# Kernel optimization log

Measured on AMD Instinct MI355X. Metric: run time of the kernel, lower is better.

The kernel has to match this reference:

```python
import jax, jax.numpy as jnp
import numpy as np

EPS = 1e-5

def setup_inputs() -> dict:
    key = jax.random.key(0)
    kx, kq, kp = jax.random.split(key, 3)
    B, T, d = 4, 4096, 512
    x = jax.random.normal(kx, (B, T, d), dtype=jnp.float32)
    mask = jnp.tril(jnp.ones((T, T), dtype=jnp.int32))  # causal 0/1 mask
    gamma = jnp.ones((d,), dtype=jnp.float32)
    beta = jnp.zeros((d,), dtype=jnp.float32)
    Wqkv = jax.random.normal(kq, (d, 3 * d), dtype=jnp.float32) / np.sqrt(d)
    Wproj = jax.random.normal(kp, (d, d), dtype=jnp.float32) / np.sqrt(d)
    return {"x": x, "mask": mask, "gamma": gamma, "beta": beta, "Wqkv": Wqkv, "Wproj": Wproj}

def reference(x, mask, gamma, beta, Wqkv, Wproj):
    B, T, C = x.shape
    # LayerNorm over last dim
    mu = jnp.mean(x, axis=-1, keepdims=True)
    var = jnp.mean(jnp.square(x - mu), axis=-1, keepdims=True)
    xn = (x - mu) * jax.lax.rsqrt(var + EPS) * gamma + beta
    # QKV projection (no bias)
    qkv = xn @ Wqkv  # [B,T,3C]
    q, k, v = jnp.split(qkv, 3, axis=-1)
    scale = 1.0 / np.sqrt(C)
    dist = jnp.einsum('btc,bsc->bts', q, k) * scale  # [B,T,T]
    dist = jnp.where(mask[:T, :T] == 0, -jnp.inf, dist)
    attn = jax.nn.softmax(dist, axis=-1)
    out = jnp.einsum('bts,bsc->btc', attn, v)
    return out @ Wproj
```

## Files before the change

kernel.cpp:

```cpp
#include <hip/hip_runtime.h>

typedef short bf16x8 __attribute__((ext_vector_type(8)));
typedef float f32x4 __attribute__((ext_vector_type(4)));

#define AS1 __attribute__((address_space(1)))
#define AS3 __attribute__((address_space(3)))

__device__ __forceinline__ void async16(const void* g, void* l) {
    __builtin_amdgcn_global_load_lds((AS1 unsigned*)(unsigned long long)g,
                                     (AS3 unsigned*)l, 16, 0, 0);
}

__device__ __forceinline__ unsigned short f2bf(float f) {
    unsigned u = __builtin_bit_cast(unsigned, f);
    u += 0x7fffu + ((u >> 16) & 1u);
    return (unsigned short)(u >> 16);
}
__device__ __forceinline__ float bf2f(unsigned short s) {
    unsigned u = ((unsigned)s) << 16;
    return __builtin_bit_cast(float, u);
}

__global__ __launch_bounds__(256) void ln_bf16_kernel(
    const float* __restrict__ x, const float* __restrict__ gamma,
    const float* __restrict__ beta, unsigned short* __restrict__ xn, int nrows)
{
    int row = blockIdx.x * 4 + (threadIdx.x >> 6);
    int lane = threadIdx.x & 63;
    if (row >= nrows) return;
    const float4* xr = (const float4*)(x + (size_t)row * 512);
    float4 a = xr[lane], b = xr[lane + 64];
    float s = a.x + a.y + a.z + a.w + b.x + b.y + b.z + b.w;
    #pragma unroll
    for (int m = 1; m < 64; m <<= 1) s += __shfl_xor(s, m);
    float mu = s * (1.0f / 512.0f);
    float dx[8] = {a.x - mu, a.y - mu, a.z - mu, a.w - mu,
                   b.x - mu, b.y - mu, b.z - mu, b.w - mu};
    float ss = 0.f;
    #pragma unroll
    for (int i = 0; i < 8; ++i) ss += dx[i] * dx[i];
    #pragma unroll
    for (int m = 1; m < 64; m <<= 1) ss += __shfl_xor(ss, m);
    float rstd = rsqrtf(ss * (1.0f / 512.0f) + 1e-5f);
    const float4* gp = (const float4*)gamma;
    const float4* bp = (const float4*)beta;
    float4 g0 = gp[lane], g1 = gp[lane + 64], b0 = bp[lane], b1 = bp[lane + 64];
    float y[8];
    y[0] = dx[0] * rstd * g0.x + b0.x; y[1] = dx[1] * rstd * g0.y + b0.y;
    y[2] = dx[2] * rstd * g0.z + b0.z; y[3] = dx[3] * rstd * g0.w + b0.w;
    y[4] = dx[4] * rstd * g1.x + b1.x; y[5] = dx[5] * rstd * g1.y + b1.y;
    y[6] = dx[6] * rstd * g1.z + b1.z; y[7] = dx[7] * rstd * g1.w + b1.w;
    ushort4* orow = (ushort4*)(xn + (size_t)row * 512);
    orow[lane]      = make_ushort4(f2bf(y[0]), f2bf(y[1]), f2bf(y[2]), f2bf(y[3]));
    orow[lane + 64] = make_ushort4(f2bf(y[4]), f2bf(y[5]), f2bf(y[6]), f2bf(y[7]));
}

__global__ __launch_bounds__(256) void transpose_w(
    const float* __restrict__ in, unsigned short* __restrict__ outT, int R, int Cd)
{
    __shared__ float tile[64][65];
    int r0 = blockIdx.x * 64, c0 = blockIdx.y * 64;
    int lr = threadIdx.x >> 6, lc = threadIdx.x & 63;
    #pragma unroll
    for (int i = 0; i < 16; ++i) {
        int r = i * 4 + lr;
        tile[r][lc] = in[(size_t)(r0 + r) * Cd + c0 + lc];
    }
    __syncthreads();
    #pragma unroll
    for (int i = 0; i < 16; ++i) {
        int r = i * 4 + lr;
        outT[(size_t)(c0 + r) * R + r0 + lc] = f2bf(tile[lc][r]);
    }
}

__global__ __launch_bounds__(256) void transpose_v(
    const unsigned short* __restrict__ vraw, unsigned short* __restrict__ vtp)
{
    __shared__ unsigned short tile[64][72];
    int b = blockIdx.z;
    int t0 = blockIdx.x * 64, c0 = blockIdx.y * 64;
    int lr = threadIdx.x >> 6, lc = threadIdx.x & 63;
    const unsigned short* src = vraw + (size_t)(b * 4096 + t0) * 512 + c0;
    #pragma unroll
    for (int i = 0; i < 16; ++i) {
        int r = i * 4 + lr;
        tile[r][lc] = src[(size_t)r * 512 + lc];
    }
    __syncthreads();
    #pragma unroll
    for (int i = 0; i < 16; ++i) {
        int r = i * 4 + lr;
        int c = c0 + r;
        int jt = (t0 >> 5) + (lc >> 5);
        int tl = lc & 31;
        int x = tl >> 3;
        int slot = c * 4 + ((x ^ (c >> 1)) & 3);
        vtp[((size_t)(b * 128 + jt)) * 16384 + slot * 8 + (tl & 7)] = tile[lc][r];
    }
}

__global__ __launch_bounds__(256) void gemm_bt(
    const unsigned short* __restrict__ A, const unsigned short* __restrict__ Bt,
    void* __restrict__ Cp, int M, int N, int K, int lda, int ldb, int ldc, int outBf16)
{
    __shared__ unsigned short As[128 * 64];
    __shared__ unsigned short Bs[128 * 64];
    const int tid = threadIdx.x;
    const int w = tid >> 6, lane = tid & 63, quad = lane >> 4, l15 = lane & 15;
    const int wm = w >> 1, wn = w & 1;
    const size_t m0 = (size_t)blockIdx.x * 128, n0 = (size_t)blockIdx.y * 128;
    f32x4 zero = {0.f, 0.f, 0.f, 0.f};
    f32x4 acc[4][4];
    #pragma unroll
    for (int i = 0; i < 4; ++i)
        #pragma unroll
        for (int j = 0; j < 4; ++j) acc[i][j] = zero;

    for (int k0 = 0; k0 < K; k0 += 64) {
        __syncthreads();
        #pragma unroll
        for (int r = 0; r < 4; ++r) {
            int s = r * 256 + w * 64 + lane;
            int row = s >> 3, x = s & 7, g = x ^ (row & 7);
            async16(A + (m0 + row) * lda + k0 + g * 8,
                    (char*)As + (size_t)(r * 256 + w * 64) * 16);
        }
        #pragma unroll
        for (int r = 0; r < 4; ++r) {
            int s = r * 256 + w * 64 + lane;
            int row = s >> 3, x = s & 7, g = x ^ (row & 7);
            async16(Bt + (n0 + row) * ldb + k0 + g * 8,
                    (char*)Bs + (size_t)(r * 256 + w * 64) * 16);
        }
        __syncthreads();
        #pragma unroll
        for (int ks = 0; ks < 2; ++ks) {
            bf16x8 af[4], bf[4];
            int cc = ks * 4 + quad;
            #pragma unroll
            for (int mt = 0; mt < 4; ++mt) {
                int row = wm * 64 + mt * 16 + l15;
                int x = cc ^ (row & 7);
                af[mt] = *(const bf16x8*)(As + row * 64 + x * 8);
            }
            #pragma unroll
            for (int nt = 0; nt < 4; ++nt) {
                int row = wn * 64 + nt * 16 + l15;
                int x = cc ^ (row & 7);
                bf[nt] = *(const bf16x8*)(Bs + row * 64 + x * 8);
            }
            #pragma unroll
            for (int mt = 0; mt < 4; ++mt)
                #pragma unroll
                for (int nt = 0; nt < 4; ++nt)
                    acc[mt][nt] = __builtin_amdgcn_mfma_f32_16x16x32_bf16(
                        af[mt], bf[nt], acc[mt][nt], 0, 0, 0);
        }
    }
    #pragma unroll
    for (int mt = 0; mt < 4; ++mt)
        #pragma unroll
        for (int nt = 0; nt < 4; ++nt)
            #pragma unroll
            for (int r = 0; r < 4; ++r) {
                size_t grow = m0 + wm * 64 + mt * 16 + quad * 4 + r;
                size_t gcol = n0 + wn * 64 + nt * 16 + l15;
                float v = acc[mt][nt][r];
                if (outBf16) ((unsigned short*)Cp)[grow * ldc + gcol] = f2bf(v);
                else         ((float*)Cp)[grow * ldc + gcol] = v;
            }
}

__global__ __launch_bounds__(256, 2) void attn_kernel(
    const unsigned short* __restrict__ qk,
    const unsigned short* __restrict__ vtp,
    unsigned short* __restrict__ ph0, unsigned short* __restrict__ ph1,
    float* __restrict__ lp)
{
    __shared__ unsigned short Ks[32 * 512];
    __shared__ unsigned short Vs[32 * 512];
    unsigned short* Ps = Ks;

    const int id = blockIdx.x;
    const int cu = id & 255, hi = id >> 8;
    const int b = cu & 3;
    const int q = hi ? (63 - (cu >> 2)) : (cu >> 2);
    const int h = hi;

    const int jt0 = h ? (q + 1) : 0;
    const int jtN = h ? (2 * q + 2) : (q + 1);

    const int tid = threadIdx.x, w = tid >> 6, lane = tid & 63;
    const int quad = lane >> 4, l15 = lane & 15;
    const float scale = 0.04419417382415922f;
    f32x4 zero = {0.f, 0.f, 0.f, 0.f};

    const unsigned short* kbase = qk + (size_t)(b * 4096) * 1024 + 512;
    const unsigned short* vbase = vtp + (size_t)(b * 128) * 16384;
    unsigned short* dst = h ? ph1 : ph0;

    bf16x8 qf[16];
    {
        const unsigned short* qb =
            qk + (size_t)(b * 4096 + q * 64 + w * 16 + l15) * 1024;
        #pragma unroll
        for (int ks = 0; ks < 16; ++ks)
            qf[ks] = *(const bf16x8*)(qb + ks * 32 + quad * 8);
    }
    f32x4 o[32];
    #pragma unroll
    for (int i = 0; i < 32; ++i) o[i] = zero;
    float li[4] = {0.f, 0.f, 0.f, 0.f};

    for (int jt = jt0; jt < jtN; ++jt) {
        __syncthreads();
        {
            const unsigned short* kg = kbase + (size_t)jt * 32 * 1024;
            #pragma unroll
            for (int rnd = 0; rnd < 8; ++rnd) {
                int s = rnd * 256 + tid;
                int row = s >> 6, xx = s & 63;
                int g = (xx & ~7) | ((xx ^ row) & 7);
                async16(kg + (size_t)row * 1024 + g * 8,
                        (char*)Ks + (size_t)(rnd * 256 + w * 64) * 16);
            }
            const unsigned short* vg = vbase + (size_t)jt * 16384;
            #pragma unroll
            for (int rnd = 0; rnd < 8; ++rnd) {
                int s = rnd * 256 + tid;
                async16(vg + (size_t)s * 8,
                        (char*)Vs + (size_t)(rnd * 256 + w * 64) * 16);
            }
        }
        __syncthreads();

        f32x4 sa[2];
        sa[0] = zero; sa[1] = zero;
        #pragma unroll
        for (int ks = 0; ks < 16; ++ks) {
            int cc = ks * 4 + quad;
            #pragma unroll
            for (int nt = 0; nt < 2; ++nt) {
                int jr = nt * 16 + l15;
                int xg = (cc & ~7) | ((cc ^ jr) & 7);
                bf16x8 kf = *(const bf16x8*)(Ks + jr * 512 + xg * 8);
                sa[nt] = __builtin_amdgcn_mfma_f32_16x16x32_bf16(
                    qf[ks], kf, sa[nt], 0, 0, 0);
            }
        }
        const int trow = q * 64 + w * 16 + quad * 4;
        unsigned short pb[4][2];
        #pragma unroll
        for (int r = 0; r < 4; ++r) {
            #pragma unroll
            for (int nt = 0; nt < 2; ++nt) {
                int col = jt * 32 + nt * 16 + l15;
                float sv = sa[nt][r] * scale;
                float pv = __expf(fminf(sv, 60.f));
                if (col > trow + r) pv = 0.f;
                li[r] += pv;
                pb[r][nt] = f2bf(pv);
            }
        }
        __syncthreads();
        #pragma unroll
        for (int r = 0; r < 4; ++r)
            #pragma unroll
            for (int nt = 0; nt < 2; ++nt)
                Ps[w * 640 + (quad * 4 + r) * 40 + nt * 16 + l15] = pb[r][nt];

        bf16x8 pf = *(const bf16x8*)(Ps + w * 640 + l15 * 40 + quad * 8);
        #pragma unroll
        for (int ct = 0; ct < 32; ++ct) {
            int cch = ct * 16 + l15;
            int slot = cch * 4 + ((quad ^ (cch >> 1)) & 3);
            bf16x8 vf = *(const bf16x8*)(Vs + slot * 8);
            o[ct] = __builtin_amdgcn_mfma_f32_16x16x32_bf16(pf, vf, o[ct], 0, 0, 0);
        }
    }

    #pragma unroll
    for (int r = 0; r < 4; ++r) {
        float s = li[r];
        s += __shfl_xor(s, 1);
        s += __shfl_xor(s, 2);
        s += __shfl_xor(s, 4);
        s += __shfl_xor(s, 8);
        if (l15 == 0)
            lp[h * 16384 + b * 4096 + q * 64 + w * 16 + quad * 4 + r] = s;
    }
    unsigned short* ob = dst + (size_t)(b * 4096 + q * 64 + w * 16) * 512;
    #pragma unroll
    for (int ct = 0; ct < 32; ++ct)
        #pragma unroll
        for (int r = 0; r < 4; ++r)
            ob[(size_t)(quad * 4 + r) * 512 + ct * 16 + l15] = f2bf(o[ct][r]);
}

__global__ __launch_bounds__(256) void combine_kernel(
    const unsigned short* __restrict__ ph0, const unsigned short* __restrict__ ph1,
    const float* __restrict__ lp, unsigned short* __restrict__ att)
{
    int t = blockIdx.x * 4 + (threadIdx.x >> 6);
    int lane = threadIdx.x & 63;
    float inv = 1.0f / (lp[t] + lp[16384 + t]);
    const ushort4* pa = (const ushort4*)(ph0 + (size_t)t * 512 + lane * 8);
    const ushort4* pb = (const ushort4*)(ph1 + (size_t)t * 512 + lane * 8);
    ushort4* po = (ushort4*)(att + (size_t)t * 512 + lane * 8);
    #pragma unroll
    for (int i = 0; i < 2; ++i) {
        ushort4 a = pa[i], b = pb[i];
        po[i] = make_ushort4(
            f2bf((bf2f(a.x) + bf2f(b.x)) * inv),
            f2bf((bf2f(a.y) + bf2f(b.y)) * inv),
            f2bf((bf2f(a.z) + bf2f(b.z)) * inv),
            f2bf((bf2f(a.w) + bf2f(b.w)) * inv));
    }
}

extern "C" void kernel_launch(void* const* d_in, const int* in_sizes, int n_in,
                              void* d_out, int out_size, void* d_ws, size_t ws_size,
                              hipStream_t stream)
{
    const float* x     = (const float*)d_in[0];
    const float* gamma = (const float*)d_in[2];
    const float* beta  = (const float*)d_in[3];
    const float* Wqkv  = (const float*)d_in[4];
    const float* Wproj = (const float*)d_in[5];
    float* out = (float*)d_out;

    char* ws = (char*)d_ws;
    unsigned short* qk     = (unsigned short*)(ws);
    unsigned short* vraw   = (unsigned short*)(ws + 33554432);
    unsigned short* vtp    = (unsigned short*)(ws + 50331648);
    unsigned short* xn     = (unsigned short*)(ws + 67108864);
    unsigned short* wqkvT  = (unsigned short*)(ws + 83886080);
    unsigned short* wprojT = (unsigned short*)(ws + 85458944);
    unsigned short* ph0    = xn;
    unsigned short* ph1    = vraw;
    float*          lp     = (float*)wqkvT;
    unsigned short* att    = vtp;

    ln_bf16_kernel<<<4096, 256, 0, stream>>>(x, gamma, beta, xn, 16384);
    transpose_w<<<dim3(8, 24), 256, 0, stream>>>(Wqkv, wqkvT, 512, 1536);
    transpose_w<<<dim3(8, 8), 256, 0, stream>>>(Wproj, wprojT, 512, 512);
    gemm_bt<<<dim3(128, 8), 256, 0, stream>>>(xn, wqkvT, qk,
                                              16384, 1024, 512, 512, 512, 1024, 1);
    gemm_bt<<<dim3(128, 4), 256, 0, stream>>>(xn, wqkvT + 1024 * 512, vraw,
                                              16384, 512, 512, 512, 512, 512, 1);
    transpose_v<<<dim3(64, 8, 4), 256, 0, stream>>>(vraw, vtp);
    attn_kernel<<<512, 256, 0, stream>>>(qk, vtp, ph0, ph1, lp);
    combine_kernel<<<4096, 256, 0, stream>>>(ph0, ph1, lp, att);
    gemm_bt<<<dim3(128, 4), 256, 0, stream>>>(att, wprojT, out,
                                              16384, 512, 512, 512, 512, 512, 0);
}
```

Measured before the change: 396.2 us.

## Restructure attention into 128-row tiles with 4-way KV split and double-buffered LDS

Rewrites the attention kernel to use 512-thread blocks that each handle a 128-query tile. The key range is split into four parts, and each block processes two work items chosen by reversed indexing to balance the causal load. K and V tiles are double-buffered, so async loads of the next tile overlap compute on the current one. The PV product is split across waves by output column rather than by query row, which cuts per-wave accumulator registers. The combine kernel now sums four partial outputs and uses the output buffer as scratch, adding memory traffic and relying on the final GEMM to overwrite it.

After: 436.9 us. 10.3% more time.

```diff
diff --git a/kernel.cpp b/kernel.cpp
--- a/kernel.cpp
+++ b/kernel.cpp
@@ -172,150 +172,172 @@
             }
 }
 
-__global__ __launch_bounds__(256, 2) void attn_kernel(
+__global__ __launch_bounds__(512, 2) void attn_kernel(
     const unsigned short* __restrict__ qk,
     const unsigned short* __restrict__ vtp,
     unsigned short* __restrict__ ph0, unsigned short* __restrict__ ph1,
+    unsigned short* __restrict__ ph2, unsigned short* __restrict__ ph3,
     float* __restrict__ lp)
 {
-    __shared__ unsigned short Ks[32 * 512];
-    __shared__ unsigned short Vs[32 * 512];
-    unsigned short* Ps = Ks;
-
-    const int id = blockIdx.x;
-    const int cu = id & 255, hi = id >> 8;
-    const int b = cu & 3;
-    const int q = hi ? (63 - (cu >> 2)) : (cu >> 2);
-    const int h = hi;
-
-    const int jt0 = h ? (q + 1) : 0;
-    const int jtN = h ? (2 * q + 2) : (q + 1);
+    __shared__ unsigned short Ks[2][32 * 512];
+    __shared__ unsigned short Vs[2][32 * 512];
+    __shared__ unsigned short Ps[128 * 40];
 
     const int tid = threadIdx.x, w = tid >> 6, lane = tid & 63;
     const int quad = lane >> 4, l15 = lane & 15;
     const float scale = 0.04419417382415922f;
     f32x4 zero = {0.f, 0.f, 0.f, 0.f};
 
-    const unsigned short* kbase = qk + (size_t)(b * 4096) * 1024 + 512;
-    const unsigned short* vbase = vtp + (size_t)(b * 128) * 16384;
-    unsigned short* dst = h ? ph1 : ph0;
-
-    bf16x8 qf[16];
-    {
-        const unsigned short* qb =
-            qk + (size_t)(b * 4096 + q * 64 + w * 16 + l15) * 1024;
-        #pragma unroll
-        for (int ks = 0; ks < 16; ++ks)
-            qf[ks] = *(const bf16x8*)(qb + ks * 32 + quad * 8);
-    }
-    f32x4 o[32];
-    #pragma unroll
-    for (int i = 0; i < 32; ++i) o[i] = zero;
-    float li[4] = {0.f, 0.f, 0.f, 0.f};
-
-    for (int jt = jt0; jt < jtN; ++jt) {
+    #pragma unroll 1
+    for (int half = 0; half < 2; ++half) {
+        const int j = half ? (511 - (int)blockIdx.x) : (int)blockIdx.x;
+        const int q = 31 - (j >> 4);
+        const int b = (j >> 2) & 3;
+        const int part = j & 3;
+        const int ntile = q + 1;
+        const int jt0 = part * ntile, jtN = jt0 + ntile;
+
+        const unsigned short* kbase = qk + (size_t)(b * 4096) * 1024 + 512;
+        const unsigned short* vbase = vtp + (size_t)(b * 128) * 16384;
+
+        bf16x8 qf[16];
+        {
+            const unsigned short* qb =
+                qk + (size_t)(b * 4096 + q * 128 + w * 16 + l15) * 1024;
+            #pragma unroll
+            for (int ks = 0; ks < 16; ++ks)
+                qf[ks] = *(const bf16x8*)(qb + ks * 32 + quad * 8);
+        }
+        f32x4 o[8][4];
+        #pragma unroll
+        for (int i = 0; i < 8; ++i)
+            #pragma unroll
+            for (int d = 0; d < 4; ++d) o[i][d] = zero;
+        float li[4] = {0.f, 0.f, 0.f, 0.f};
+
+        #define STAGE(BUF, T)                                                     \
+        {                                                                         \
+            const unsigned short* kg = kbase + (size_t)(T) * 32 * 1024;           \
+            _Pragma("unroll")                                                     \
+            for (int rnd = 0; rnd < 4; ++rnd) {                                   \
+                int s = rnd * 512 + tid;                                          \
+                int row = s >> 6, xx = s & 63;                                    \
+                int g = (xx & ~7) | ((xx ^ row) & 7);                             \
+                async16(kg + (size_t)row * 1024 + g * 8,                          \
+                        (char*)(&Ks[BUF][0]) + (size_t)(rnd * 512 + w * 64) * 16);\
+            }                                                                     \
+            const unsigned short* vg = vbase + (size_t)(T) * 16384;               \
+            _Pragma("unroll")                                                     \
+            for (int rnd = 0; rnd < 4; ++rnd) {                                   \
+                int s = rnd * 512 + tid;                                          \
+                async16(vg + (size_t)s * 8,                                       \
+                        (char*)(&Vs[BUF][0]) + (size_t)(rnd * 512 + w * 64) * 16);\
+            }                                                                     \
+        }
+
+        STAGE(0, jt0);
         __syncthreads();
-        {
-            const unsigned short* kg = kbase + (size_t)jt * 32 * 1024;
-            #pragma unroll
-            for (int rnd = 0; rnd < 8; ++rnd) {
-                int s = rnd * 256 + tid;
-                int row = s >> 6, xx = s & 63;
-                int g = (xx & ~7) | ((xx ^ row) & 7);
-                async16(kg + (size_t)row * 1024 + g * 8,
-                        (char*)Ks + (size_t)(rnd * 256 + w * 64) * 16);
-            }
-            const unsigned short* vg = vbase + (size_t)jt * 16384;
-            #pragma unroll
-            for (int rnd = 0; rnd < 8; ++rnd) {
-                int s = rnd * 256 + tid;
-                async16(vg + (size_t)s * 8,
-                        (char*)Vs + (size_t)(rnd * 256 + w * 64) * 16);
-            }
-        }
-        __syncthreads();
-
-        f32x4 sa[2];
-        sa[0] = zero; sa[1] = zero;
-        #pragma unroll
-        for (int ks = 0; ks < 16; ++ks) {
-            int cc = ks * 4 + quad;
-            #pragma unroll
-            for (int nt = 0; nt < 2; ++nt) {
-                int jr = nt * 16 + l15;
-                int xg = (cc & ~7) | ((cc ^ jr) & 7);
-                bf16x8 kf = *(const bf16x8*)(Ks + jr * 512 + xg * 8);
-                sa[nt] = __builtin_amdgcn_mfma_f32_16x16x32_bf16(
-                    qf[ks], kf, sa[nt], 0, 0, 0);
-            }
-        }
-        const int trow = q * 64 + w * 16 + quad * 4;
-        unsigned short pb[4][2];
+        int cur = 0;
+
+        #pragma unroll 1
+        for (int t = jt0; t < jtN; ++t) {
+            if (t + 1 < jtN) STAGE(cur ^ 1, t + 1);
+
+            f32x4 sa[2];
+            sa[0] = zero; sa[1] = zero;
+            #pragma unroll
+            for (int ks = 0; ks < 16; ++ks) {
+                int cc = ks * 4 + quad;
+                #pragma unroll
+                for (int nt = 0; nt < 2; ++nt) {
+                    int jr = nt * 16 + l15;
+                    int xg = (cc & ~7) | ((cc ^ jr) & 7);
+                    bf16x8 kf = *(const bf16x8*)(&Ks[cur][jr * 512 + xg * 8]);
+                    sa[nt] = __builtin_amdgcn_mfma_f32_16x16x32_bf16(
+                        qf[ks], kf, sa[nt], 0, 0, 0);
+                }
+            }
+            const int trow = q * 128 + w * 16 + quad * 4;
+            #pragma unroll
+            for (int r = 0; r < 4; ++r) {
+                #pragma unroll
+                for (int nt = 0; nt < 2; ++nt) {
+                    int col = t * 32 + nt * 16 + l15;
+                    float sv = sa[nt][r] * scale;
+                    float pv = __expf(fminf(sv, 60.f));
+                    if (col > trow + r) pv = 0.f;
+                    li[r] += pv;
+                    Ps[(w * 16 + quad * 4 + r) * 40 + nt * 16 + l15] = f2bf(pv);
+                }
+            }
+            asm volatile("s_waitcnt lgkmcnt(0)" ::: "memory");
+            __builtin_amdgcn_s_barrier();
+
+            bf16x8 vfr[4];
+            #pragma unroll
+            for (int df = 0; df < 4; ++df) {
+                int cch = (w * 4 + df) * 16 + l15;
+                int slot = cch * 4 + ((quad ^ (cch >> 1)) & 3);
+                vfr[df] = *(const bf16x8*)(&Vs[cur][slot * 8]);
+            }
+            #pragma unroll
+            for (int qi = 0; qi < 8; ++qi) {
+                bf16x8 pa = *(const bf16x8*)(&Ps[(qi * 16 + l15) * 40 + quad * 8]);
+                #pragma unroll
+                for (int df = 0; df < 4; ++df)
+                    o[qi][df] = __builtin_amdgcn_mfma_f32_16x16x32_bf16(
+                        pa, vfr[df], o[qi][df], 0, 0, 0);
+            }
+            __syncthreads();
+            cur ^= 1;
+        }
+        #undef STAGE
+
         #pragma unroll
         for (int r = 0; r < 4; ++r) {
-            #pragma unroll
-            for (int nt = 0; nt < 2; ++nt) {
-                int col = jt * 32 + nt * 16 + l15;
-                float sv = sa[nt][r] * scale;
-                float pv = __expf(fminf(sv, 60.f));
-                if (col > trow + r) pv = 0.f;
-                li[r] += pv;
-                pb[r][nt] = f2bf(pv);
-            }
-        }
-        __syncthreads();
-        #pragma unroll
-        for (int r = 0; r < 4; ++r)
-            #pragma unroll
-            for (int nt = 0; nt < 2; ++nt)
-                Ps[w * 640 + (quad * 4 + r) * 40 + nt * 16 + l15] = pb[r][nt];
-
-        bf16x8 pf = *(const bf16x8*)(Ps + w * 640 + l15 * 40 + quad * 8);
-        #pragma unroll
-        for (int ct = 0; ct < 32; ++ct) {
-            int cch = ct * 16 + l15;
-            int slot = cch * 4 + ((quad ^ (cch >> 1)) & 3);
-            bf16x8 vf = *(const bf16x8*)(Vs + slot * 8);
-            o[ct] = __builtin_amdgcn_mfma_f32_16x16x32_bf16(pf, vf, o[ct], 0, 0, 0);
-        }
-    }
-
-    #pragma unroll
-    for (int r = 0; r < 4; ++r) {
-        float s = li[r];
-        s += __shfl_xor(s, 1);
-        s += __shfl_xor(s, 2);
-        s += __shfl_xor(s, 4);
-        s += __shfl_xor(s, 8);
-        if (l15 == 0)
-            lp[h * 16384 + b * 4096 + q * 64 + w * 16 + quad * 4 + r] = s;
-    }
-    unsigned short* ob = dst + (size_t)(b * 4096 + q * 64 + w * 16) * 512;
-    #pragma unroll
-    for (int ct = 0; ct < 32; ++ct)
-        #pragma unroll
-        for (int r = 0; r < 4; ++r)
-            ob[(size_t)(quad * 4 + r) * 512 + ct * 16 + l15] = f2bf(o[ct][r]);
+            float s = li[r];
+            s += __shfl_xor(s, 1);
+            s += __shfl_xor(s, 2);
+            s += __shfl_xor(s, 4);
+            s += __shfl_xor(s, 8);
+            if (l15 == 0)
+                lp[part * 16384 + b * 4096 + q * 128 + w * 16 + quad * 4 + r] = s;
+        }
+        unsigned short* dst = (part == 0) ? ph0 : (part == 1) ? ph1
+                            : (part == 2) ? ph2 : ph3;
+        unsigned short* ob = dst + (size_t)(b * 4096 + q * 128) * 512 + w * 64;
+        #pragma unroll
+        for (int qi = 0; qi < 8; ++qi)
+            #pragma unroll
+            for (int df = 0; df < 4; ++df)
+                #pragma unroll
+                for (int r = 0; r < 4; ++r)
+                    ob[(size_t)(qi * 16 + quad * 4 + r) * 512 + df * 16 + l15] =
+                        f2bf(o[qi][df][r]);
+    }
 }
 
 __global__ __launch_bounds__(256) void combine_kernel(
     const unsigned short* __restrict__ ph0, const unsigned short* __restrict__ ph1,
+    const unsigned short* __restrict__ ph2, const unsigned short* __restrict__ ph3,
     const float* __restrict__ lp, unsigned short* __restrict__ att)
 {
     int t = blockIdx.x * 4 + (threadIdx.x >> 6);
     int lane = threadIdx.x & 63;
-    float inv = 1.0f / (lp[t] + lp[16384 + t]);
+    float inv = 1.0f / (lp[t] + lp[16384 + t] + lp[32768 + t] + lp[49152 + t]);
     const ushort4* pa = (const ushort4*)(ph0 + (size_t)t * 512 + lane * 8);
     const ushort4* pb = (const ushort4*)(ph1 + (size_t)t * 512 + lane * 8);
+    const ushort4* pc = (const ushort4*)(ph2 + (size_t)t * 512 + lane * 8);
+    const ushort4* pd = (const ushort4*)(ph3 + (size_t)t * 512 + lane * 8);
     ushort4* po = (ushort4*)(att + (size_t)t * 512 + lane * 8);
     #pragma unroll
     for (int i = 0; i < 2; ++i) {
-        ushort4 a = pa[i], b = pb[i];
+        ushort4 a = pa[i], b = pb[i], c = pc[i], d = pd[i];
         po[i] = make_ushort4(
-            f2bf((bf2f(a.x) + bf2f(b.x)) * inv),
-            f2bf((bf2f(a.y) + bf2f(b.y)) * inv),
-            f2bf((bf2f(a.z) + bf2f(b.z)) * inv),
-            f2bf((bf2f(a.w) + bf2f(b.w)) * inv));
+            f2bf((bf2f(a.x) + bf2f(b.x) + bf2f(c.x) + bf2f(d.x)) * inv),
+            f2bf((bf2f(a.y) + bf2f(b.y) + bf2f(c.y) + bf2f(d.y)) * inv),
+            f2bf((bf2f(a.z) + bf2f(b.z) + bf2f(c.z) + bf2f(d.z)) * inv),
+            f2bf((bf2f(a.w) + bf2f(b.w) + bf2f(c.w) + bf2f(d.w)) * inv));
     }
 }
 
@@ -339,6 +361,8 @@
     unsigned short* wprojT = (unsigned short*)(ws + 85458944);
     unsigned short* ph0    = xn;
     unsigned short* ph1    = vraw;
+    unsigned short* ph2    = (unsigned short*)out;
+    unsigned short* ph3    = (unsigned short*)out + (size_t)16384 * 512;
     float*          lp     = (float*)wqkvT;
     unsigned short* att    = vtp;
 
@@ -350,8 +374,8 @@
     gemm_bt<<<dim3(128, 4), 256, 0, stream>>>(xn, wqkvT + 1024 * 512, vraw,
                                               16384, 512, 512, 512, 512, 512, 1);
     transpose_v<<<dim3(64, 8, 4), 256, 0, stream>>>(vraw, vtp);
-    attn_kernel<<<512, 256, 0, stream>>>(qk, vtp, ph0, ph1, lp);
-    combine_kernel<<<4096, 256, 0, stream>>>(ph0, ph1, lp, att);
+    attn_kernel<<<256, 512, 0, stream>>>(qk, vtp, ph0, ph1, ph2, ph3, lp);
+    combine_kernel<<<4096, 256, 0, stream>>>(ph0, ph1, ph2, ph3, lp, att);
     gemm_bt<<<dim3(128, 4), 256, 0, stream>>>(att, wprojT, out,
                                               16384, 512, 512, 512, 512, 512, 0);
 }
```

## Repartition PV matmul so each wave owns a head-dim slice across all query rows

Applied to the files above, without the earlier changes.

The P·V stage is reorganised so each wave computes a 128-wide slice of the output dimension for all 64 query rows, instead of all 512 columns for its own 16 rows. This lets each wave load only a quarter of the V tile from LDS and reuse each V fragment across four P fragments. P therefore moves to its own shared buffer visible to every wave, with a barrier after it is written, and the old reuse of the K buffer plus the extra pre-write sync is dropped. K/V async-load address math is also hoisted out of the loop. The cost is more LDS, which may affect the two-blocks-per-CU occupancy target.

Result: faster. 362.6 us (-8.5%).

```diff
diff --git a/kernel.cpp b/kernel.cpp
--- a/kernel.cpp
+++ b/kernel.cpp
@@ -180,7 +180,7 @@
 {
     __shared__ unsigned short Ks[32 * 512];
     __shared__ unsigned short Vs[32 * 512];
-    unsigned short* Ps = Ks;
+    __shared__ unsigned short Ps[64 * 40];
 
     const int id = blockIdx.x;
     const int cu = id & 255, hi = id >> 8;
@@ -200,6 +200,12 @@
     const unsigned short* vbase = vtp + (size_t)(b * 128) * 16384;
     unsigned short* dst = h ? ph1 : ph0;
 
+    const int gE = (lane & ~7) | ((lane ^ w) & 7);
+    const int gO = (lane & ~7) | ((lane ^ (w + 4)) & 7);
+    const size_t kOffE = (size_t)w * 1024 + (size_t)gE * 8;
+    const size_t kOffO = (size_t)(w + 4) * 1024 + (size_t)gO * 8;
+    const size_t vOff  = (size_t)tid * 8;
+
     bf16x8 qf[16];
     {
         const unsigned short* qb =
@@ -208,30 +214,29 @@
         for (int ks = 0; ks < 16; ++ks)
             qf[ks] = *(const bf16x8*)(qb + ks * 32 + quad * 8);
     }
-    f32x4 o[32];
-    #pragma unroll
-    for (int i = 0; i < 32; ++i) o[i] = zero;
+    f32x4 o[4][8];
+    #pragma unroll
+    for (int i = 0; i < 4; ++i)
+        #pragma unroll
+        for (int d = 0; d < 8; ++d) o[i][d] = zero;
     float li[4] = {0.f, 0.f, 0.f, 0.f};
 
     for (int jt = jt0; jt < jtN; ++jt) {
         __syncthreads();
         {
-            const unsigned short* kg = kbase + (size_t)jt * 32 * 1024;
-            #pragma unroll
-            for (int rnd = 0; rnd < 8; ++rnd) {
-                int s = rnd * 256 + tid;
-                int row = s >> 6, xx = s & 63;
-                int g = (xx & ~7) | ((xx ^ row) & 7);
-                async16(kg + (size_t)row * 1024 + g * 8,
-                        (char*)Ks + (size_t)(rnd * 256 + w * 64) * 16);
-            }
-            const unsigned short* vg = vbase + (size_t)jt * 16384;
-            #pragma unroll
-            for (int rnd = 0; rnd < 8; ++rnd) {
-                int s = rnd * 256 + tid;
-                async16(vg + (size_t)s * 8,
+            const unsigned short* kg = kbase + (size_t)jt * 32768;
+            #pragma unroll
+            for (int rr = 0; rr < 4; ++rr) {
+                async16(kg + (size_t)(2 * rr) * 4096 + kOffE,
+                        (char*)Ks + (size_t)((2 * rr) * 256 + w * 64) * 16);
+                async16(kg + (size_t)(2 * rr) * 4096 + kOffO,
+                        (char*)Ks + (size_t)((2 * rr + 1) * 256 + w * 64) * 16);
+            }
+            const unsigned short* vg = vbase + (size_t)jt * 16384 + vOff;
+            #pragma unroll
+            for (int rnd = 0; rnd < 8; ++rnd)
+                async16(vg + (size_t)rnd * 2048,
                         (char*)Vs + (size_t)(rnd * 256 + w * 64) * 16);
-            }
         }
         __syncthreads();
 
@@ -250,7 +255,6 @@
             }
         }
         const int trow = q * 64 + w * 16 + quad * 4;
-        unsigned short pb[4][2];
         #pragma unroll
         for (int r = 0; r < 4; ++r) {
             #pragma unroll
@@ -260,23 +264,29 @@
                 float pv = __expf(fminf(sv, 60.f));
                 if (col > trow + r) pv = 0.f;
                 li[r] += pv;
-                pb[r][nt] = f2bf(pv);
-            }
-        }
-        __syncthreads();
-        #pragma unroll
-        for (int r = 0; r < 4; ++r)
-            #pragma unroll
-            for (int nt = 0; nt < 2; ++nt)
-                Ps[w * 640 + (quad * 4 + r) * 40 + nt * 16 + l15] = pb[r][nt];
-
-        bf16x8 pf = *(const bf16x8*)(Ps + w * 640 + l15 * 40 + quad * 8);
-        #pragma unroll
-        for (int ct = 0; ct < 32; ++ct) {
-            int cch = ct * 16 + l15;
-            int slot = cch * 4 + ((quad ^ (cch >> 1)) & 3);
-            bf16x8 vf = *(const bf16x8*)(Vs + slot * 8);
-            o[ct] = __builtin_amdgcn_mfma_f32_16x16x32_bf16(pf, vf, o[ct], 0, 0, 0);
+                Ps[(w * 16 + quad * 4 + r) * 40 + nt * 16 + l15] = f2bf(pv);
+            }
+        }
+        asm volatile("s_waitcnt lgkmcnt(0)" ::: "memory");
+        __builtin_amdgcn_s_barrier();
+
+        #pragma unroll
+        for (int ph = 0; ph < 2; ++ph) {
+            bf16x8 vfr[4];
+            #pragma unroll
+            for (int d4 = 0; d4 < 4; ++d4) {
+                int cch = (w * 8 + ph * 4 + d4) * 16 + l15;
+                int slot = cch * 4 + ((quad ^ (cch >> 1)) & 3);
+                vfr[d4] = *(const bf16x8*)(Vs + slot * 8);
+            }
+            #pragma unroll
+            for (int qi = 0; qi < 4; ++qi) {
+                bf16x8 pa = *(const bf16x8*)(Ps + (qi * 16 + l15) * 40 + quad * 8);
+                #pragma unroll
+                for (int d4 = 0; d4 < 4; ++d4)
+                    o[qi][ph * 4 + d4] = __builtin_amdgcn_mfma_f32_16x16x32_bf16(
+                        pa, vfr[d4], o[qi][ph * 4 + d4], 0, 0, 0);
+            }
         }
     }
 
@@ -290,12 +300,15 @@
         if (l15 == 0)
             lp[h * 16384 + b * 4096 + q * 64 + w * 16 + quad * 4 + r] = s;
     }
-    unsigned short* ob = dst + (size_t)(b * 4096 + q * 64 + w * 16) * 512;
-    #pragma unroll
-    for (int ct = 0; ct < 32; ++ct)
-        #pragma unroll
-        for (int r = 0; r < 4; ++r)
-            ob[(size_t)(quad * 4 + r) * 512 + ct * 16 + l15] = f2bf(o[ct][r]);
+    unsigned short* ob = dst + (size_t)(b * 4096 + q * 64) * 512 + w * 128;
+    #pragma unroll
+    for (int qi = 0; qi < 4; ++qi)
+        #pragma unroll
+        for (int df = 0; df < 8; ++df)
+            #pragma unroll
+            for (int r = 0; r < 4; ++r)
+                ob[(size_t)(qi * 16 + quad * 4 + r) * 512 + df * 16 + l15] =
+                    f2bf(o[qi][df][r]);
 }
 
 __global__ __launch_bounds__(256) void combine_kernel(
```
